# Performance work log

Hardware: AMD Instinct MI355X
Metric: run time of the kernel (lower is better)

The kernel has to match this reference:

```python
import jax, jax.numpy as jnp
import numpy as np

B, T, D = 2, 2048, 1024
H, d = 16, 64
INNER = H * d
K = 4  # conv_size
EPS_RMS = 1e-6
EPS_NORM = 1e-12


def _dconv(x, w, b):
    # depthwise causal conv: x (B,T,C), w (C,K), b (C,)
    xp = jnp.pad(x, ((0, 0), (K - 1, 0), (0, 0)))
    Tt = x.shape[1]
    out = b
    for k in range(K):
        out = out + xp[:, k:k + Tt] * w[:, k]
    return out


def _l2norm(x):
    n = jnp.sqrt(jnp.sum(x * x, axis=-1, keepdims=True))
    return x / jnp.maximum(n, EPS_NORM)


def setup_inputs() -> dict:
    key = jax.random.key(0)
    ks = jax.random.split(key, 12)
    s = 0.02
    inp = {
        'x': jax.random.normal(ks[0], (B, T, D), jnp.float32),
        'Wq': jax.random.normal(ks[1], (D, INNER), jnp.float32) * s,
        'Wk': jax.random.normal(ks[2], (D, INNER), jnp.float32) * s,
        'Wv': jax.random.normal(ks[3], (D, INNER), jnp.float32) * s,
        'Wa': jax.random.normal(ks[4], (D, H), jnp.float32) * s,
        'ba': jnp.full((H,), 2.0, jnp.float32),
        'Wb': jax.random.normal(ks[5], (D, H), jnp.float32) * s,
        'bb': jnp.zeros((H,), jnp.float32),
        'Wg': jax.random.normal(ks[6], (D, INNER), jnp.float32) * s,
        'Wo': jax.random.normal(ks[7], (INNER, D), jnp.float32) * s,
        'cq_w': jax.random.normal(ks[8], (INNER, K), jnp.float32) * 0.3,
        'cq_b': jnp.zeros((INNER,), jnp.float32),
        'ck_w': jax.random.normal(ks[9], (INNER, K), jnp.float32) * 0.3,
        'ck_b': jnp.zeros((INNER,), jnp.float32),
        'cv_w': jax.random.normal(ks[10], (INNER, K), jnp.float32) * 0.3,
        'cv_b': jnp.zeros((INNER,), jnp.float32),
        'gamma': jnp.zeros((INNER,), jnp.float32),
    }
    return inp


def reference(x, Wq, Wk, Wv, Wa, ba, Wb, bb, Wg, Wo,
              cq_w, cq_b, ck_w, ck_b, cv_w, cv_b, gamma):
    q = jax.nn.silu(_dconv(x @ Wq, cq_w, cq_b))
    k = jax.nn.silu(_dconv(x @ Wk, ck_w, ck_b))
    v = jax.nn.silu(_dconv(x @ Wv, cv_w, cv_b))
    q = _l2norm(q.reshape(B, T, H, d))
    k = _l2norm(k.reshape(B, T, H, d))
    v = v.reshape(B, T, H, d)
    alpha = jax.nn.sigmoid(x @ Wa + ba)  # (B,T,H)
    beta = jax.nn.sigmoid(x @ Wb + bb)   # (B,T,H)
    gate = jax.nn.silu(x @ Wg)           # (B,T,INNER)

    I_d = jnp.eye(d, dtype=x.dtype)

    def step(S, ins):
        q_t, k_t, v_t, a_t, b_t = ins  # q/k/v: (B,H,d); a,b: (B,H)
        a = a_t[..., None, None]
        b = b_t[..., None, None]
        kkT = k_t[..., :, None] * k_t[..., None, :]   # (B,H,d,d)
        vkT = v_t[..., :, None] * k_t[..., None, :]
        decay = a * (I_d - b * kkT)
        S = jnp.matmul(S, decay) + b * vkT
        o = jnp.einsum('bhde,bhe->bhd', S, q_t)
        return S, o

    # time-major scan inputs
    qT = jnp.transpose(q, (1, 0, 2, 3))
    kT = jnp.transpose(k, (1, 0, 2, 3))
    vT = jnp.transpose(v, (1, 0, 2, 3))
    aT = jnp.transpose(alpha, (1, 0, 2))
    bT = jnp.transpose(beta, (1, 0, 2))
    S0 = jnp.zeros((B, H, d, d), x.dtype)
    _, oT = jax.lax.scan(step, S0, (qT, kT, vT, aT, bT))  # (T,B,H,d)

    out = jnp.transpose(oT, (1, 0, 2, 3)).reshape(B, T, INNER)
    rms = jnp.sqrt(jnp.mean(out * out, axis=-1, keepdims=True) + EPS_RMS)
    out = out / rms * (1.0 + gamma)
    out = out * gate
    return out @ Wo
```

## Files before the change

kernel.cpp:

```cpp
#include <hip/hip_runtime.h>
#include <hip/hip_bf16.h>
#include <cmath>

#define B_ 2
#define T_ 2048
#define D_ 1024
#define H_ 16
#define DH 64
#define INNER_ 1024
#define BT (B_*T_)
#define NCH 32
#define NU (B_*H_*NCH)
#define N1 ((size_t)BT * INNER_)

typedef __attribute__((ext_vector_type(8))) __bf16 bf16x8;
typedef __attribute__((ext_vector_type(4))) float f32x4;
typedef const __attribute__((address_space(1))) unsigned gas_u32;
typedef __attribute__((address_space(3))) unsigned las_u32;

__device__ __forceinline__ void async16(const void* g, void* l) {
  __builtin_amdgcn_global_load_lds((gas_u32*)g, (las_u32*)l, 16, 0, 0);
}

__device__ __forceinline__ ushort bfr(float x) {
  __hip_bfloat16 t = __float2bfloat16(x);
  return *(ushort*)&t;
}
__device__ __forceinline__ void st_bf4(__hip_bfloat16* p, float a, float b, float c, float d) {
  ushort4 u; u.x = bfr(a); u.y = bfr(b); u.z = bfr(c); u.w = bfr(d);
  *(ushort4*)p = u;
}
__device__ __forceinline__ float b2f(ushort s) {
  return __uint_as_float(((unsigned)s) << 16);
}

__global__ __launch_bounds__(256) void prep_kernel(
    const float* __restrict__ x,
    const float* __restrict__ Wq, const float* __restrict__ Wk,
    const float* __restrict__ Wv, const float* __restrict__ Wg,
    const float* __restrict__ Wo, const float* __restrict__ Wa,
    const float* __restrict__ Wb,
    __hip_bfloat16* __restrict__ xb, __hip_bfloat16* __restrict__ wtall,
    __hip_bfloat16* __restrict__ Wot) {
  __shared__ float tile[32][33];
  const int bid = blockIdx.x, tid = threadIdx.x;
  if (bid < 4096) {
    int i = bid * 256 + tid;
    float4 v = *(const float4*)(x + (size_t)i * 4);
    st_bf4(xb + (size_t)i * 4, v.x, v.y, v.z, v.w);
    return;
  }
  if (bid < 9216) {
    int wi = (bid - 4096) >> 10;
    int t = (bid - 4096) & 1023;
    const float* src = wi == 0 ? Wq : wi == 1 ? Wk : wi == 2 ? Wv : wi == 3 ? Wg : Wo;
    __hip_bfloat16* dst = (wi < 4) ? (wtall + (size_t)wi * 1024 * 1024) : Wot;
    const int bc = (t & 31) * 32, br = (t >> 5) * 32;
    const int tx = tid & 31, ty = tid >> 5;
#pragma unroll
    for (int i2 = 0; i2 < 32; i2 += 8)
      tile[ty + i2][tx] = src[(size_t)(br + ty + i2) * 1024 + bc + tx];
    __syncthreads();
#pragma unroll
    for (int i2 = 0; i2 < 32; i2 += 8)
      dst[(size_t)(bc + ty + i2) * 1024 + br + tx] = __float2bfloat16(tile[tx][ty + i2]);
    return;
  }
  int idx = (bid - 9216) * 256 + tid;
  int j = idx >> 10, k2 = idx & 1023;
  float v = 0.f;
  if (j < 16) v = Wa[k2 * 16 + j];
  else if (j < 32) v = Wb[k2 * 16 + (j - 16)];
  wtall[(size_t)4096 * 1024 + idx] = __float2bfloat16(v);
}

__device__ __forceinline__ bf16x8 pfrag(const __hip_bfloat16* buf, int row, int ks, int lg) {
  return *(const bf16x8*)((const char*)buf + row * 128 + ks * 64 + lg * 16);
}

__global__ __launch_bounds__(512, 2) void gemm256(const __hip_bfloat16* __restrict__ A,
                                                  const __hip_bfloat16* __restrict__ Bt,
                                                  float* __restrict__ Cf,
                                                  __hip_bfloat16* __restrict__ Cb,
                                                  float* __restrict__ alpha,
                                                  float* __restrict__ beta,
                                                  const float* __restrict__ ba,
                                                  const float* __restrict__ bb2,
                                                  int M, int N, int K, int act) {
  __shared__ __hip_bfloat16 As[2][256 * 64];
  __shared__ __hip_bfloat16 Bs[2][256 * 64];
  const int tid = threadIdx.x;
  const int lane = tid & 63, wv = tid >> 6;
  const int wr = wv >> 2, wc = wv & 3;
  const int m0 = blockIdx.y * 256, n0 = blockIdx.x * 256;
  const int l15 = lane & 15, lg = lane >> 4;
  const int sr8 = lane >> 3, sc = (lane & 7) * 8;

  f32x4 acc[8][4];
#pragma unroll
  for (int m = 0; m < 8; ++m)
#pragma unroll
    for (int n = 0; n < 4; ++n) acc[m][n] = (f32x4)0.f;

  auto stage = [&](int kt, int bsel) {
    const size_t k0 = (size_t)kt * 64;
    const __hip_bfloat16* Ab = A + (size_t)(m0 + wv * 8 + sr8) * K + k0 + sc;
    const __hip_bfloat16* Bb = Bt + (size_t)(n0 + wv * 8 + sr8) * K + k0 + sc;
    char* al = (char*)As[bsel] + wv * 1024;
    char* bl = (char*)Bs[bsel] + wv * 1024;
#pragma unroll
    for (int q = 0; q < 4; ++q) {
      async16(Ab + (size_t)q * 64 * K, al + q * 8192);
      async16(Bb + (size_t)q * 64 * K, bl + q * 8192);
    }
  };

  const int NT = K >> 6;
  stage(0, 0);
  __syncthreads();
  int cur = 0;
  for (int kt = 0; kt < NT; ++kt) {
    if (kt + 1 < NT) stage(kt + 1, cur ^ 1);
#pragma unroll
    for (int ks = 0; ks < 2; ++ks) {
      bf16x8 af[8], bfg[4];
#pragma unroll
      for (int m = 0; m < 8; ++m)
        af[m] = pfrag(As[cur], wr * 128 + m * 16 + l15, ks, lg);
#pragma unroll
      for (int n = 0; n < 4; ++n)
        bfg[n] = pfrag(Bs[cur], wc * 64 + n * 16 + l15, ks, lg);
#pragma unroll
      for (int m = 0; m < 8; ++m)
#pragma unroll
        for (int n = 0; n < 4; ++n)
          acc[m][n] = __builtin_amdgcn_mfma_f32_16x16x32_bf16(af[m], bfg[n], acc[m][n], 0, 0, 0);
    }
    __syncthreads();
    cur ^= 1;
  }

#pragma unroll
  for (int m = 0; m < 8; ++m) {
    const int rbase = m0 + wr * 128 + m * 16 + lg * 4;
#pragma unroll
    for (int n = 0; n < 4; ++n) {
      const int col = n0 + wc * 64 + n * 16 + l15;
      if (act == 2) {
        if (col < 4096) {
          const int which = col >> 10;
          const int ncol = col & 1023;
          __hip_bfloat16* dst = Cb + (size_t)which * N1 + (size_t)rbase * 1024 + ncol;
#pragma unroll
          for (int r = 0; r < 4; ++r) {
            float vv = acc[m][n][r];
            if (which == 3) vv = vv / (1.f + expf(-vv));
            dst[(size_t)r * 1024] = __float2bfloat16(vv);
          }
        } else {
          const int ncol = col - 4096;
          if (ncol < 32) {
            const float bias = (ncol < 16) ? ba[ncol] : bb2[ncol - 16];
            float* dst = (ncol < 16) ? (alpha + ncol) : (beta + (ncol - 16));
#pragma unroll
            for (int r = 0; r < 4; ++r)
              dst[(size_t)(rbase + r) * H_] = 1.f / (1.f + expf(-(acc[m][n][r] + bias)));
          }
        }
      } else {
#pragma unroll
        for (int r = 0; r < 4; ++r)
          Cf[(size_t)(rbase + r) * N + col] = acc[m][n][r];
      }
    }
  }
}

#define BST 72

__device__ __forceinline__ bf16x8 fragld(const __hip_bfloat16* buf, int row, int kk, int lg) {
  return *(const bf16x8*)(buf + row * BST + kk * 32 + lg * 8);
}

__global__ __launch_bounds__(256, 2) void precomp_kernel(
    const __hip_bfloat16* __restrict__ qpre, const __hip_bfloat16* __restrict__ kpre,
    const __hip_bfloat16* __restrict__ vpre,
    const float* __restrict__ alpha, const float* __restrict__ beta,
    const float* __restrict__ cqw, const float* __restrict__ cqb,
    const float* __restrict__ ckw, const float* __restrict__ ckb,
    const float* __restrict__ cvw, const float* __restrict__ cvb,
    __hip_bfloat16* __restrict__ Zg, __hip_bfloat16* __restrict__ G2g,
    float* __restrict__ AVg, float* __restrict__ G1g, float* __restrict__ P63g) {
  __shared__ __hip_bfloat16 sKb[64 * BST], sKip[64 * BST], sKipT[64 * BST];
  __shared__ __hip_bfloat16 sQp[64 * BST], sAttn[64 * BST];
  __shared__ __hip_bfloat16 sXT[128 * BST];
  __shared__ __hip_bfloat16 sM[64 * BST];
  __shared__ float sMd[4][16][16];
  __shared__ float sP[64], sIP[64], sBP[64], sB[64];

  const int u = blockIdx.x;
  const int bh = u >> 5, c = u & 31;
  const int b = bh >> 4, h = bh & 15;
  const int tid = threadIdx.x, lane = tid & 63, wv = tid >> 6;
  const int l15 = lane & 15, lg = lane >> 4;
  const size_t bt0 = (size_t)b * T_ + (size_t)c * 64;
  const size_t hofs = (size_t)h * DH;

  if (wv == 0) {
    float a = alpha[(bt0 + lane) * H_ + h];
    float bb = beta[(bt0 + lane) * H_ + h];
    float la = logf(a);
#pragma unroll
    for (int d = 1; d < 64; d <<= 1) {
      float y = __shfl_up(la, d);
      if (lane >= d) la += y;
    }
    float P = expf(la);
    sP[lane] = P;
    sIP[lane] = 1.f / P;
    sBP[lane] = bb * P;
    sB[lane] = bb;
    if (lane == 63) P63g[u] = P;
  }
  __syncthreads();

#pragma unroll
  for (int i = 0; i < 4; ++i) {
    int e = tid + i * 256;
    int row = e >> 4, c4 = (e & 15) * 4;
    int gc = (int)hofs + c4;
    int tseq = c * 64 + row;
    float rq[4], rk[4], rv[4];
    {
      float4 bq = *(const float4*)(cqb + gc);
      float4 bk = *(const float4*)(ckb + gc);
      float4 bv = *(const float4*)(cvb + gc);
      rq[0] = bq.x; rq[1] = bq.y; rq[2] = bq.z; rq[3] = bq.w;
      rk[0] = bk.x; rk[1] = bk.y; rk[2] = bk.z; rk[3] = bk.w;
      rv[0] = bv.x; rv[1] = bv.y; rv[2] = bv.z; rv[3] = bv.w;
    }
    float wq[4][4], wk[4][4], wvv[4][4];
#pragma unroll
    for (int j = 0; j < 4; ++j) {
      float4 a4 = *(const float4*)(cqw + (size_t)(gc + j) * 4);
      wq[j][0] = a4.x; wq[j][1] = a4.y; wq[j][2] = a4.z; wq[j][3] = a4.w;
      float4 b4 = *(const float4*)(ckw + (size_t)(gc + j) * 4);
      wk[j][0] = b4.x; wk[j][1] = b4.y; wk[j][2] = b4.z; wk[j][3] = b4.w;
      float4 c4v = *(const float4*)(cvw + (size_t)(gc + j) * 4);
      wvv[j][0] = c4v.x; wvv[j][1] = c4v.y; wvv[j][2] = c4v.z; wvv[j][3] = c4v.w;
    }
#pragma unroll
    for (int kk = 0; kk < 4; ++kk) {
      if (tseq - 3 + kk >= 0) {
        size_t off = (bt0 + row - 3 + kk) * INNER_ + gc;
        ushort4 uq = *(const ushort4*)(qpre + off);
        ushort4 uk = *(const ushort4*)(kpre + off);
        ushort4 uv = *(const ushort4*)(vpre + off);
        rq[0] += b2f(uq.x) * wq[0][kk]; rq[1] += b2f(uq.y) * wq[1][kk];
        rq[2] += b2f(uq.z) * wq[2][kk]; rq[3] += b2f(uq.w) * wq[3][kk];
        rk[0] += b2f(uk.x) * wk[0][kk]; rk[1] += b2f(uk.y) * wk[1][kk];
        rk[2] += b2f(uk.z) * wk[2][kk]; rk[3] += b2f(uk.w) * wk[3][kk];
        rv[0] += b2f(uv.x) * wvv[0][kk]; rv[1] += b2f(uv.y) * wvv[1][kk];
        rv[2] += b2f(uv.z) * wvv[2][kk]; rv[3] += b2f(uv.w) * wvv[3][kk];
      }
    }
#pragma unroll
    for (int j = 0; j < 4; ++j) {
      rq[j] = rq[j] / (1.f + expf(-rq[j]));
      rk[j] = rk[j] / (1.f + expf(-rk[j]));
      rv[j] = rv[j] / (1.f + expf(-rv[j]));
    }
    float ssq = rq[0]*rq[0] + rq[1]*rq[1] + rq[2]*rq[2] + rq[3]*rq[3];
    float ssk = rk[0]*rk[0] + rk[1]*rk[1] + rk[2]*rk[2] + rk[3]*rk[3];
    ssq += __shfl_xor(ssq, 1); ssq += __shfl_xor(ssq, 2);
    ssq += __shfl_xor(ssq, 4); ssq += __shfl_xor(ssq, 8);
    ssk += __shfl_xor(ssk, 1); ssk += __shfl_xor(ssk, 2);
    ssk += __shfl_xor(ssk, 4); ssk += __shfl_xor(ssk, 8);
    float scq = 1.f / fmaxf(sqrtf(ssq), 1e-12f);
    float sck = 1.f / fmaxf(sqrtf(ssk), 1e-12f);
#pragma unroll
    for (int j = 0; j < 4; ++j) { rq[j] *= scq; rk[j] *= sck; }

    float bp = sBP[row], ip = sIP[row], pp = sP[row], bo = sB[row];
    st_bf4(&sKb[row * BST + c4], rk[0] * bp, rk[1] * bp, rk[2] * bp, rk[3] * bp);
    st_bf4(&sKip[row * BST + c4], rk[0] * ip, rk[1] * ip, rk[2] * ip, rk[3] * ip);
    st_bf4(&sQp[row * BST + c4], rq[0] * pp, rq[1] * pp, rq[2] * pp, rq[3] * pp);
#pragma unroll
    for (int j = 0; j < 4; ++j) {
      sKipT[(c4 + j) * BST + row] = __float2bfloat16(rk[j] * ip);
      sXT[(c4 + j) * BST + row] = __float2bfloat16(rk[j] * bp);
      sXT[(64 + c4 + j) * BST + row] = __float2bfloat16(rv[j] * bo);
    }
  }
  __syncthreads();

  if (wv < 2) {
#pragma unroll
    for (int tt = wv * 2; tt < wv * 2 + 2; ++tt) {
      for (int n = 0; n <= tt; ++n) {
        f32x4 acc = (f32x4)0.f;
#pragma unroll
        for (int kk = 0; kk < 2; ++kk)
          acc = __builtin_amdgcn_mfma_f32_16x16x32_bf16(
              fragld(sKb, tt * 16 + l15, kk, lg), fragld(sKip, n * 16 + l15, kk, lg), acc, 0, 0, 0);
        if (n < tt) {
#pragma unroll
          for (int q = 0; q < 4; ++q)
            sM[(tt * 16 + lg * 4 + q) * BST + n * 16 + l15] = __float2bfloat16(acc[q]);
        } else {
#pragma unroll
          for (int q = 0; q < 4; ++q) {
            int rr = lg * 4 + q;
            sMd[tt][rr][l15] = (l15 < rr) ? acc[q] : 0.f;
            sM[(tt * 16 + rr) * BST + tt * 16 + l15] = __float2bfloat16(0.f);
          }
        }
      }
    }
  } else {
#pragma unroll
    for (int tt = (wv - 2) * 2; tt < (wv - 2) * 2 + 2; ++tt) {
      for (int n = 0; n < 4; ++n) {
        if (n <= tt) {
          f32x4 acc = (f32x4)0.f;
#pragma unroll
          for (int kk = 0; kk < 2; ++kk)
            acc = __builtin_amdgcn_mfma_f32_16x16x32_bf16(
                fragld(sQp, tt * 16 + l15, kk, lg), fragld(sKip, n * 16 + l15, kk, lg), acc, 0, 0, 0);
#pragma unroll
          for (int q = 0; q < 4; ++q) {
            int r = tt * 16 + lg * 4 + q, cl = n * 16 + l15;
            sAttn[r * BST + cl] = __float2bfloat16((cl <= r) ? acc[q] : 0.f);
          }
        } else {
#pragma unroll
          for (int q = 0; q < 4; ++q)
            sAttn[(tt * 16 + lg * 4 + q) * BST + n * 16 + l15] = __float2bfloat16(0.f);
        }
      }
    }
  }
  __syncthreads();

  auto diag_solve = [&](int I) {
    if (wv < 2) {
      const int cc = wv * 64 + lane;
      float x[16];
#pragma unroll
      for (int t = 0; t < 16; ++t) {
        float r = __bfloat162float(sXT[cc * BST + I * 16 + t]);
#pragma unroll
        for (int s = 0; s < t; ++s) r -= sMd[I][t][s] * x[s];
        x[t] = r;
        sXT[cc * BST + I * 16 + t] = __float2bfloat16(r);
      }
    }
  };

  diag_solve(0);
  __syncthreads();
#pragma unroll
  for (int I = 1; I < 4; ++I) {
    const int KK = (I == 3) ? 2 : 1;
#pragma unroll
    for (int ct2 = 0; ct2 < 2; ++ct2) {
      const int ct = wv * 2 + ct2;
      f32x4 uacc = (f32x4)0.f;
#pragma unroll
      for (int kk = 0; kk < KK; ++kk)
        uacc = __builtin_amdgcn_mfma_f32_16x16x32_bf16(
            fragld(sXT, ct * 16 + l15, kk, lg), fragld(sM, I * 16 + l15, kk, lg), uacc, 0, 0, 0);
#pragma unroll
      for (int q = 0; q < 4; ++q) {
        const int cc = ct * 16 + lg * 4 + q, t = I * 16 + l15;
        float old = __bfloat162float(sXT[cc * BST + t]);
        sXT[cc * BST + t] = __float2bfloat16(old - uacc[q]);
      }
    }
    __syncthreads();
    diag_solve(I);
    __syncthreads();
  }

  const float p63 = sP[63];
  const int tt = wv;
  const size_t go = (size_t)u * 4096;
#pragma unroll
  for (int n = 0; n < 4; ++n) {
    f32x4 av = (f32x4)0.f, aw = (f32x4)0.f, g1 = (f32x4)0.f, g2 = (f32x4)0.f;
#pragma unroll
    for (int kk = 0; kk < 2; ++kk) {
      bf16x8 at = fragld(sAttn, tt * 16 + l15, kk, lg);
      bf16x8 kt = fragld(sKipT, tt * 16 + l15, kk, lg);
      bf16x8 bv = fragld(sXT, 64 + n * 16 + l15, kk, lg);
      bf16x8 bw = fragld(sXT, n * 16 + l15, kk, lg);
      av = __builtin_amdgcn_mfma_f32_16x16x32_bf16(at, bv, av, 0, 0, 0);
      aw = __builtin_amdgcn_mfma_f32_16x16x32_bf16(at, bw, aw, 0, 0, 0);
      g1 = __builtin_amdgcn_mfma_f32_16x16x32_bf16(kt, bv, g1, 0, 0, 0);
      g2 = __builtin_amdgcn_mfma_f32_16x16x32_bf16(kt, bw, g2, 0, 0, 0);
    }
#pragma unroll
    for (int q = 0; q < 4; ++q) {
      int r = tt * 16 + lg * 4 + q, cl = n * 16 + l15;
      AVg[go + r * 64 + cl] = av[q];
      float qp = __bfloat162float(sQp[r * BST + cl]);
      Zg[go + r * 64 + cl] = __float2bfloat16(qp - aw[q]);
      G1g[go + cl * 64 + r] = p63 * g1[q];
      G2g[go + r * 64 + cl] = __float2bfloat16(p63 * g2[q]);
    }
  }
}

__device__ __forceinline__ bf16x8 sfrag(const __hip_bfloat16* buf, int row, int kk, int lg) {
  int byte = row * 128 + kk * 64 + lg * 16;
  byte ^= (row & 7) << 4;
  return *(const bf16x8*)((const char*)buf + byte);
}

__global__ __launch_bounds__(256) void chunkrec_kernel(
    const __hip_bfloat16* __restrict__ Zg, const __hip_bfloat16* __restrict__ G2g,
    const float* __restrict__ AVg, const float* __restrict__ G1g,
    const float* __restrict__ P63g, float* __restrict__ o) {
  __shared__ __align__(16) __hip_bfloat16 sR[16 * 64];
  __shared__ __align__(16) __hip_bfloat16 sZ[2][64 * 64];
  __shared__ __align__(16) __hip_bfloat16 sG2[2][64 * 64];
  const int blk = blockIdx.x;
  const int bh = blk >> 2;
  const int jb = blk & 3;
  const int b = bh >> 4, h = bh & 15;
  const int tid = threadIdx.x, lane = tid & 63, wv = tid >> 6;
  const int l15 = lane & 15, lg = lane >> 4;
  const size_t btb = (size_t)b * T_;
  const size_t hofs = (size_t)h * DH;

  f32x4 R = (f32x4)0.f;

  uint4 zr[2], gr[2];
  const int e0 = tid * 2;

  auto issue = [&](int c) {
    size_t ub = ((size_t)bh * NCH + c) * 4096;
#pragma unroll
    for (int i = 0; i < 2; ++i) {
      zr[i] = *(const uint4*)(Zg + ub + (size_t)(e0 + i) * 8);
      gr[i] = *(const uint4*)(G2g + ub + (size_t)(e0 + i) * 8);
    }
  };
  auto commit = [&](int buf) {
#pragma unroll
    for (int i = 0; i < 2; ++i) {
      int e = e0 + i;
      int row = e >> 3, colb = (e & 7) * 16;
      int byte = (row * 128 + colb) ^ ((row & 7) << 4);
      *(uint4*)((char*)sZ[buf] + byte) = zr[i];
      *(uint4*)((char*)sG2[buf] + byte) = gr[i];
    }
  };

  issue(0);
  commit(0);
  int cur = 0;
  for (int c = 0; c < NCH; ++c) {
#pragma unroll
    for (int q = 0; q < 4; ++q) {
      int i = lg * 4 + q;
      int byte = (i * 128 + (wv * 16 + l15) * 2) ^ ((i & 7) << 4);
      *(__hip_bfloat16*)((char*)sR + byte) = __float2bfloat16(R[q]);
    }
    __syncthreads();

    const size_t ub = ((size_t)bh * NCH + c) * 4096;
    float avr[4], g1r[4];
#pragma unroll
    for (int q = 0; q < 4; ++q) {
      int t = wv * 16 + lg * 4 + q;
      avr[q] = AVg[ub + t * 64 + jb * 16 + l15];
      g1r[q] = G1g[ub + (jb * 16 + lg * 4 + q) * 64 + wv * 16 + l15];
    }
    float p63 = P63g[(size_t)bh * NCH + c];
    if (c + 1 < NCH) issue(c + 1);

    bf16x8 zA[2], rF[2], gB[2];
#pragma unroll
    for (int kk = 0; kk < 2; ++kk) {
      zA[kk] = sfrag(sZ[cur], wv * 16 + l15, kk, lg);
      rF[kk] = sfrag(sR, l15, kk, lg);
      gB[kk] = sfrag(sG2[cur], wv * 16 + l15, kk, lg);
    }
    f32x4 oacc = (f32x4)0.f, gacc = (f32x4)0.f;
#pragma unroll
    for (int kk = 0; kk < 2; ++kk) {
      oacc = __builtin_amdgcn_mfma_f32_16x16x32_bf16(zA[kk], rF[kk], oacc, 0, 0, 0);
      gacc = __builtin_amdgcn_mfma_f32_16x16x32_bf16(rF[kk], gB[kk], gacc, 0, 0, 0);
    }
#pragma unroll
    for (int q = 0; q < 4; ++q) {
      int t = wv * 16 + lg * 4 + q;
      o[(btb + (size_t)c * 64 + t) * INNER_ + hofs + jb * 16 + l15] = avr[q] + oacc[q];
      R[q] = p63 * R[q] + g1r[q] - gacc[q];
    }
    __syncthreads();
    if (c + 1 < NCH) commit(cur ^ 1);
    cur ^= 1;
  }
}

__global__ __launch_bounds__(256) void rmsgate_kernel(const float* __restrict__ o,
    const __hip_bfloat16* __restrict__ gate, const float* __restrict__ gamma,
    __hip_bfloat16* __restrict__ outn) {
  const int bt = blockIdx.x;
  const int tid = threadIdx.x;
  const size_t base = (size_t)bt * INNER_ + tid * 4;
  float4 ov = *(const float4*)(o + base);
  float ss = ov.x*ov.x + ov.y*ov.y + ov.z*ov.z + ov.w*ov.w;
#pragma unroll
  for (int m = 1; m <= 32; m <<= 1) ss += __shfl_xor(ss, m);
  __shared__ float red[4];
  if ((tid & 63) == 0) red[tid >> 6] = ss;
  __syncthreads();
  float tot = red[0] + red[1] + red[2] + red[3];
  float rms = sqrtf(tot * (1.f / (float)INNER_) + 1e-6f);
  float inv = 1.f / rms;
  float4 gm = *(const float4*)(gamma + tid * 4);
  ushort4 gt = *(const ushort4*)(gate + base);
  st_bf4(outn + base,
         ov.x * inv * (1.f + gm.x) * b2f(gt.x),
         ov.y * inv * (1.f + gm.y) * b2f(gt.y),
         ov.z * inv * (1.f + gm.z) * b2f(gt.z),
         ov.w * inv * (1.f + gm.w) * b2f(gt.w));
}

extern "C" void kernel_launch(void* const* d_in, const int* in_sizes, int n_in,
                              void* d_out, int out_size, void* d_ws, size_t ws_size,
                              hipStream_t stream) {
  const float* x   = (const float*)d_in[0];
  const float* Wq  = (const float*)d_in[1];
  const float* Wk  = (const float*)d_in[2];
  const float* Wv  = (const float*)d_in[3];
  const float* Wa  = (const float*)d_in[4];
  const float* ba  = (const float*)d_in[5];
  const float* Wb  = (const float*)d_in[6];
  const float* bb  = (const float*)d_in[7];
  const float* Wg  = (const float*)d_in[8];
  const float* Wo  = (const float*)d_in[9];
  const float* cqw = (const float*)d_in[10];
  const float* cqb = (const float*)d_in[11];
  const float* ckw = (const float*)d_in[12];
  const float* ckb = (const float*)d_in[13];
  const float* cvw = (const float*)d_in[14];
  const float* cvb = (const float*)d_in[15];
  const float* gamma = (const float*)d_in[16];

  char* p = (char*)d_ws;
  __hip_bfloat16* qkvg = (__hip_bfloat16*)p;  p += 4 * N1 * 2;
  __hip_bfloat16* xb   = (__hip_bfloat16*)p;  p += N1 * 2;
  float* alpha = (float*)p;  p += (size_t)BT * H_ * 4;
  float* beta  = (float*)p;  p += (size_t)BT * H_ * 4;
  __hip_bfloat16* wtall = (__hip_bfloat16*)p;  p += (size_t)4352 * 1024 * 2;
  __hip_bfloat16* Wot   = (__hip_bfloat16*)p;  p += (size_t)1024 * 1024 * 2;
  float* AVg = (float*)p;  p += (size_t)NU * 4096 * 4;
  float* G1g = (float*)p;  p += (size_t)NU * 4096 * 4;
  __hip_bfloat16* Zg  = (__hip_bfloat16*)p;  p += (size_t)NU * 4096 * 2;
  __hip_bfloat16* G2g = (__hip_bfloat16*)p;  p += (size_t)NU * 4096 * 2;
  float* obuf = (float*)p;  p += N1 * 4;
  float* P63s = (float*)p;  p += (size_t)NU * 4;
  __hip_bfloat16* nrmb = xb;
  float* outp = (float*)d_out;

  prep_kernel<<<10240, 256, 0, stream>>>(x, Wq, Wk, Wv, Wg, Wo, Wa, Wb, xb, wtall, Wot);

  gemm256<<<dim3(17, BT / 256), 512, 0, stream>>>(
      xb, wtall, nullptr, qkvg, alpha, beta, ba, bb, BT, 4352, D_, 2);

  precomp_kernel<<<NU, 256, 0, stream>>>(qkvg, qkvg + N1, qkvg + 2 * N1,
                                         alpha, beta, cqw, cqb, ckw, ckb, cvw, cvb,
                                         Zg, G2g, AVg, G1g, P63s);
  chunkrec_kernel<<<B_ * H_ * 4, 256, 0, stream>>>(Zg, G2g, AVg, G1g, P63s, obuf);

  rmsgate_kernel<<<BT, 256, 0, stream>>>(obuf, qkvg + 3 * N1, gamma, nrmb);
  gemm256<<<dim3(D_ / 256, BT / 256), 512, 0, stream>>>(
      nrmb, Wot, outp, nullptr, nullptr, nullptr, nullptr, nullptr, BT, D_, INNER_, 0);
}
```

Before: 365.1 us.

## Remap QKV GEMM block order and use smaller-tile GEMM for output projection

The fused QKV/alpha/beta GEMM now uses a 1D grid with a custom block-to-tile mapping. It groups eight column tiles per row band, which may improve L2 reuse and XCD distribution, and it spreads the narrow alpha/beta column across blocks. The output projection drops the 256x256 tile kernel, which launched only 64 blocks, for a new 128x128 single-buffered GEMM with 256 blocks, giving more parallelism on the many-CU device. The new GEMM has no double buffering, so load latency may be less well hidden.

```diff
diff --git a/kernel.cpp b/kernel.cpp
--- a/kernel.cpp
+++ b/kernel.cpp
@@ -80,19 +80,25 @@
 
 __global__ __launch_bounds__(512, 2) void gemm256(const __hip_bfloat16* __restrict__ A,
                                                   const __hip_bfloat16* __restrict__ Bt,
-                                                  float* __restrict__ Cf,
                                                   __hip_bfloat16* __restrict__ Cb,
                                                   float* __restrict__ alpha,
                                                   float* __restrict__ beta,
                                                   const float* __restrict__ ba,
                                                   const float* __restrict__ bb2,
-                                                  int M, int N, int K, int act) {
+                                                  int K) {
   __shared__ __hip_bfloat16 As[2][256 * 64];
   __shared__ __hip_bfloat16 Bs[2][256 * 64];
   const int tid = threadIdx.x;
   const int lane = tid & 63, wv = tid >> 6;
   const int wr = wv >> 2, wc = wv & 3;
-  const int m0 = blockIdx.y * 256, n0 = blockIdx.x * 256;
+  int m0, n0;
+  {
+    const int i = blockIdx.x, x8 = i & 7, q = i >> 3;
+    int row, col;
+    if (q < 32) { col = x8 + 8 * (q >> 4); row = q & 15; }
+    else        { col = 16; row = (x8 << 1) | (q & 1); }
+    m0 = row * 256; n0 = col * 256;
+  }
   const int l15 = lane & 15, lg = lane >> 4;
   const int sr8 = lane >> 3, sc = (lane & 7) * 8;
 
@@ -146,32 +152,84 @@
 #pragma unroll
     for (int n = 0; n < 4; ++n) {
       const int col = n0 + wc * 64 + n * 16 + l15;
-      if (act == 2) {
-        if (col < 4096) {
-          const int which = col >> 10;
-          const int ncol = col & 1023;
-          __hip_bfloat16* dst = Cb + (size_t)which * N1 + (size_t)rbase * 1024 + ncol;
-#pragma unroll
-          for (int r = 0; r < 4; ++r) {
-            float vv = acc[m][n][r];
-            if (which == 3) vv = vv / (1.f + expf(-vv));
-            dst[(size_t)r * 1024] = __float2bfloat16(vv);
-          }
-        } else {
-          const int ncol = col - 4096;
-          if (ncol < 32) {
-            const float bias = (ncol < 16) ? ba[ncol] : bb2[ncol - 16];
-            float* dst = (ncol < 16) ? (alpha + ncol) : (beta + (ncol - 16));
-#pragma unroll
-            for (int r = 0; r < 4; ++r)
-              dst[(size_t)(rbase + r) * H_] = 1.f / (1.f + expf(-(acc[m][n][r] + bias)));
-          }
+      if (col < 4096) {
+        const int which = col >> 10;
+        const int ncol = col & 1023;
+        __hip_bfloat16* dst = Cb + (size_t)which * N1 + (size_t)rbase * 1024 + ncol;
+#pragma unroll
+        for (int r = 0; r < 4; ++r) {
+          float vv = acc[m][n][r];
+          if (which == 3) vv = vv / (1.f + expf(-vv));
+          dst[(size_t)r * 1024] = __float2bfloat16(vv);
         }
       } else {
-#pragma unroll
-        for (int r = 0; r < 4; ++r)
-          Cf[(size_t)(rbase + r) * N + col] = acc[m][n][r];
+        const int ncol = col - 4096;
+        if (ncol < 32) {
+          const float bias = (ncol < 16) ? ba[ncol] : bb2[ncol - 16];
+          float* dst = (ncol < 16) ? (alpha + ncol) : (beta + (ncol - 16));
+#pragma unroll
+          for (int r = 0; r < 4; ++r)
+            dst[(size_t)(rbase + r) * H_] = 1.f / (1.f + expf(-(acc[m][n][r] + bias)));
+        }
       }
+    }
+  }
+}
+
+__global__ __launch_bounds__(256) void gemm_bf16(const __hip_bfloat16* __restrict__ A,
+                                                 const __hip_bfloat16* __restrict__ Bt,
+                                                 float* __restrict__ C,
+                                                 int M, int N, int K) {
+  __shared__ __hip_bfloat16 As[128 * 32];
+  __shared__ __hip_bfloat16 Bs[128 * 32];
+  const int tid = threadIdx.x;
+  const int lane = tid & 63, wave = tid >> 6;
+  const int wr = wave >> 1, wc = wave & 1;
+  const int m0 = blockIdx.y * 128, n0 = blockIdx.x * 128;
+  const int srow = tid >> 2, skoff = (tid & 3) * 8;
+  const int l15 = lane & 15, lg = lane >> 4;
+
+  f32x4 acc[4][4];
+#pragma unroll
+  for (int m = 0; m < 4; ++m)
+#pragma unroll
+    for (int n = 0; n < 4; ++n) acc[m][n] = (f32x4)0.f;
+
+  char* asB = (char*)As;
+  char* bsB = (char*)Bs;
+  const int ldsw = wave * 1024;
+
+  for (int k0 = 0; k0 < K; k0 += 32) {
+    async16(A + (size_t)(m0 + srow) * K + k0 + skoff, asB + ldsw);
+    async16(A + (size_t)(m0 + 64 + srow) * K + k0 + skoff, asB + 4096 + ldsw);
+    async16(Bt + (size_t)(n0 + srow) * K + k0 + skoff, bsB + ldsw);
+    async16(Bt + (size_t)(n0 + 64 + srow) * K + k0 + skoff, bsB + 4096 + ldsw);
+    __syncthreads();
+
+    bf16x8 af[4], bfg[4];
+#pragma unroll
+    for (int m = 0; m < 4; ++m)
+      af[m] = *(const bf16x8*)(asB + ((wr * 64 + m * 16 + l15) * 32 + lg * 8) * 2);
+#pragma unroll
+    for (int n = 0; n < 4; ++n)
+      bfg[n] = *(const bf16x8*)(bsB + ((wc * 64 + n * 16 + l15) * 32 + lg * 8) * 2);
+#pragma unroll
+    for (int m = 0; m < 4; ++m)
+#pragma unroll
+      for (int n = 0; n < 4; ++n)
+        acc[m][n] = __builtin_amdgcn_mfma_f32_16x16x32_bf16(af[m], bfg[n], acc[m][n], 0, 0, 0);
+    __syncthreads();
+  }
+
+#pragma unroll
+  for (int m = 0; m < 4; ++m) {
+    const int rbase = m0 + wr * 64 + m * 16 + lg * 4;
+#pragma unroll
+    for (int n = 0; n < 4; ++n) {
+      const int col = n0 + wc * 64 + n * 16 + l15;
+#pragma unroll
+      for (int r = 0; r < 4; ++r)
+        C[(size_t)(rbase + r) * N + col] = acc[m][n][r];
     }
   }
 }
@@ -569,8 +627,7 @@
 
   prep_kernel<<<10240, 256, 0, stream>>>(x, Wq, Wk, Wv, Wg, Wo, Wa, Wb, xb, wtall, Wot);
 
-  gemm256<<<dim3(17, BT / 256), 512, 0, stream>>>(
-      xb, wtall, nullptr, qkvg, alpha, beta, ba, bb, BT, 4352, D_, 2);
+  gemm256<<<272, 512, 0, stream>>>(xb, wtall, qkvg, alpha, beta, ba, bb, D_);
 
   precomp_kernel<<<NU, 256, 0, stream>>>(qkvg, qkvg + N1, qkvg + 2 * N1,
                                          alpha, beta, cqw, cqb, ckw, ckb, cvw, cvb,
@@ -578,6 +635,5 @@
   chunkrec_kernel<<<B_ * H_ * 4, 256, 0, stream>>>(Zg, G2g, AVg, G1g, P63s, obuf);
 
   rmsgate_kernel<<<BT, 256, 0, stream>>>(obuf, qkvg + 3 * N1, gamma, nrmb);
-  gemm256<<<dim3(D_ / 256, BT / 256), 512, 0, stream>>>(
-      nrmb, Wot, outp, nullptr, nullptr, nullptr, nullptr, nullptr, BT, D_, INNER_, 0);
-}
+  gemm_bf16<<<dim3(D_ / 128, BT / 128), 256, 0, stream>>>(nrmb, Wot, outp, BT, D_, INNER_);
+}
```

New measurement: 347.4 us. 4.9% less time.
